# Optimization experiments

Hardware: AMD Instinct MI355X
Metric: run time of the kernel (lower is better)

The kernel has to match this reference:

```python
import jax, jax.numpy as jnp
import numpy as np
from jax import lax

D = 128          # dense volume side length
N = 500_000      # active voxels
CIN = 32
COUT = 32
K = 125          # 5x5x5 kernel taps
EPS = 1e-5       # BatchNorm eps (torch default)


def _build_sparse_grid():
    """Sample N unique voxels in a D^3 volume and build the [N, K] neighbor
    index table for a 5x5x5 stencil (-1 = neighbor not in the sparse grid)."""
    rng = np.random.default_rng(0)
    flat = rng.choice(D ** 3, size=N, replace=False).astype(np.int64)
    vol = np.full(D ** 3, -1, np.int32)
    vol[flat] = np.arange(N, dtype=np.int32)
    cz = flat % D
    cy = (flat // D) % D
    cx = flat // (D * D)
    coords = np.stack([cx, cy, cz], axis=1)
    nbr = np.empty((N, K), np.int32)
    k = 0
    for dx in range(-2, 3):
        for dy in range(-2, 3):
            for dz in range(-2, 3):
                c = coords + np.array([dx, dy, dz])
                ok = ((c >= 0) & (c < D)).all(axis=1)
                f = (c[:, 0] * D + c[:, 1]) * D + c[:, 2]
                nbr[:, k] = np.where(ok, vol[np.clip(f, 0, D ** 3 - 1)], -1)
                k += 1
    return nbr


def setup_inputs() -> dict:
    key = jax.random.key(0)
    ks = jax.random.split(key, 5)
    nbr = jnp.asarray(_build_sparse_grid())
    return {
        "x": jax.random.normal(ks[0], (N, CIN), jnp.float32),
        "nbr": nbr,
        "W_conv": jax.random.normal(ks[1], (K, CIN, COUT), jnp.float32) * 0.02,
        "b_conv": jax.random.normal(ks[2], (COUT,), jnp.float32) * 0.02,
        "gamma": jnp.ones((COUT,), jnp.float32),
        "beta": jnp.zeros((COUT,), jnp.float32),
        "W_lin": jax.random.normal(ks[3], (COUT, COUT), jnp.float32) * 0.02,
        "b_lin": jax.random.normal(ks[4], (COUT,), jnp.float32) * 0.02,
    }


def reference(x, nbr, W_conv, b_conv, gamma, beta, W_lin, b_lin):
    n = x.shape[0]

    # Sparse 5x5x5 conv: scan over the 125 kernel taps, gather neighbor
    # features (zero for missing neighbors) and accumulate tap GEMMs.
    def tap(acc, wi):
        w, idx = wi                              # w: [CIN, COUT], idx: [N]
        valid = (idx >= 0)[:, None]
        g = jnp.where(valid, x[jnp.maximum(idx, 0)], 0.0)  # [N, CIN]
        return acc + g @ w, None

    init = jnp.broadcast_to(b_conv, (n, b_conv.shape[0])).astype(x.dtype)
    out, _ = lax.scan(tap, init, (W_conv, nbr.T))

    # BatchNorm over all voxels (training-mode batch statistics, biased var)
    mean = out.mean(axis=0)
    var = out.var(axis=0)
    out = (out - mean) * lax.rsqrt(var + EPS) * gamma + beta

    # ELU (alpha=1.0), then pointwise SparseLinear
    out = jax.nn.elu(out)
    return out @ W_lin.T + b_lin
```

## Files before the change

### kernel.cpp

```cpp
#include <hip/hip_runtime.h>
#include <stdint.h>


#define NV 500000
#define KT 125
#define CH 32
#define EPSBN 1e-5f
#define NTILES (NV / 16)

typedef __attribute__((ext_vector_type(8))) short short8;
typedef __attribute__((ext_vector_type(4))) float f32x4;

__device__ __forceinline__ unsigned short f2bf(float f) {
    union { float f; unsigned int u; } v; v.f = f;
    unsigned int u = v.u;
    return (unsigned short)((u + 0x7fffu + ((u >> 16) & 1u)) >> 16);
}

__global__ __launch_bounds__(256) void
k_prep(const float* __restrict__ x, const float* __restrict__ Wc,
       const float* __restrict__ Wlin,
       unsigned short* __restrict__ xb, unsigned short* __restrict__ wf,
       unsigned short* __restrict__ wl, float* __restrict__ stats) {
    int tid = blockIdx.x * blockDim.x + threadIdx.x;
    if (blockIdx.x == 0 && threadIdx.x < 64) stats[threadIdx.x] = 0.0f;
    if (tid < KT * 2 * 64) {
        int k = tid >> 7;
        int rem = tid & 127;
        int h = rem >> 6;
        int l = rem & 63;
        int kd0 = (l >> 4) * 8;
        int cc = h * 16 + (l & 15);
        #pragma unroll
        for (int j = 0; j < 8; j++)
            wf[tid * 8 + j] = f2bf(Wc[(k * CH + kd0 + j) * CH + cc]);
    } else if (tid < KT * 2 * 64 + 128) {
        int t2 = tid - KT * 2 * 64;
        int h = t2 >> 6;
        int l = t2 & 63;
        int n = l & 15;
        int kd0 = (l >> 4) * 8;
        #pragma unroll
        for (int j = 0; j < 8; j++)
            wl[t2 * 8 + j] = f2bf(Wlin[(h * 16 + n) * CH + kd0 + j]);
    }
    size_t i8 = (size_t)tid * 8;
    if (i8 < (size_t)NV * CH) {
        float4 a = *(const float4*)(x + i8);
        float4 b = *(const float4*)(x + i8 + 4);
        short8 o;
        o[0] = (short)f2bf(a.x); o[1] = (short)f2bf(a.y);
        o[2] = (short)f2bf(a.z); o[3] = (short)f2bf(a.w);
        o[4] = (short)f2bf(b.x); o[5] = (short)f2bf(b.y);
        o[6] = (short)f2bf(b.z); o[7] = (short)f2bf(b.w);
        *(short8*)(xb + i8) = o;
    }
}


__device__ __forceinline__ void
load_nb(int w, const int* __restrict__ nbr, const int (&rbase)[4], int q, int (&out)[4][4]) {
    #pragma unroll
    for (int t = 0; t < 4; t++) {
        #pragma unroll
        for (int r = 0; r < 4; r++) {
            int k = w * 16 + r * 4 + q;
            out[t][r] = nbr[rbase[t] + (k > 124 ? 124 : k)];
        }
    }
}

template<int BANK, int C0>
__device__ __forceinline__ void
refill(short8 (&A)[2][2][4], short8 (&B)[2][2][2], int k0, const int (&nb)[4][4],
       const unsigned short* __restrict__ xb, const unsigned short* __restrict__ wf,
       int m, int q, int lane) {
    #pragma unroll
    for (int jj = 0; jj < 2; jj++) {
        const int c = C0 + jj;
        int k = k0 + jj;
        int kc = k > 124 ? 124 : k;
        B[BANK][jj][0] = *(const short8*)(wf + (size_t)(kc * 128 + lane) * 8);
        B[BANK][jj][1] = *(const short8*)(wf + (size_t)(kc * 128 + 64 + lane) * 8);
        #pragma unroll
        for (int t = 0; t < 4; t++) {
            int idx = __shfl(nb[t][c >> 2], ((c & 3) << 4) | m, 64);
            if (k > 124) idx = -1;
            short8 a = {0, 0, 0, 0, 0, 0, 0, 0};
            if (idx >= 0) a = *(const short8*)(xb + (size_t)idx * CH + q * 8);
            A[BANK][jj][t] = a;
        }
    }
}

template<int BANK>
__device__ __forceinline__ void
consume(f32x4 (&acc)[4][2], const short8 (&A)[2][2][4], const short8 (&B)[2][2][2]) {
    #pragma unroll
    for (int jj = 0; jj < 2; jj++) {
        #pragma unroll
        for (int t = 0; t < 4; t++) {
            acc[t][0] = __builtin_amdgcn_mfma_f32_16x16x32_bf16(A[BANK][jj][t], B[BANK][jj][0], acc[t][0], 0, 0, 0);
            acc[t][1] = __builtin_amdgcn_mfma_f32_16x16x32_bf16(A[BANK][jj][t], B[BANK][jj][1], acc[t][1], 0, 0, 0);
        }
    }
}

__global__ __launch_bounds__(256, 2) void
k_conv(const unsigned short* __restrict__ xb, const int* __restrict__ nbr,
       const unsigned short* __restrict__ wf, float* __restrict__ co,
       float* __restrict__ stats) {
    const int lane = threadIdx.x & 63;
    const int wv = threadIdx.x >> 6;
    const int m = lane & 15;
    const int q = lane >> 4;
    const int vbase = (blockIdx.x * 4 + wv) * 64;

    f32x4 acc[4][2];
    #pragma unroll
    for (int t = 0; t < 4; t++)
        for (int h = 0; h < 2; h++)
            acc[t][h] = f32x4{0.f, 0.f, 0.f, 0.f};

    bool tval[4];
    int rbase[4];
    #pragma unroll
    for (int t = 0; t < 4; t++) {
        tval[t] = (vbase + t * 16) < NV;
        rbase[t] = tval[t] ? (vbase + t * 16 + m) * KT : 0;
    }

    short8 A[2][2][4];
    short8 B[2][2][2];
    int nb[4][4], nbn[4][4];

    load_nb(0, nbr, rbase, q, nb);
    refill<0, 0>(A, B, 0, nb, xb, wf, m, q, lane);
    refill<1, 2>(A, B, 2, nb, xb, wf, m, q, lane);

    for (int w = 0; w < 8; w++) {
        const int kb = w * 16;
        if (w < 7) load_nb(w + 1, nbr, rbase, q, nbn);
        consume<0>(acc, A, B); refill<0, 4>(A, B, kb + 4, nb, xb, wf, m, q, lane);
        consume<1>(acc, A, B); refill<1, 6>(A, B, kb + 6, nb, xb, wf, m, q, lane);
        consume<0>(acc, A, B); refill<0, 8>(A, B, kb + 8, nb, xb, wf, m, q, lane);
        consume<1>(acc, A, B); refill<1, 10>(A, B, kb + 10, nb, xb, wf, m, q, lane);
        consume<0>(acc, A, B); refill<0, 12>(A, B, kb + 12, nb, xb, wf, m, q, lane);
        consume<1>(acc, A, B); refill<1, 14>(A, B, kb + 14, nb, xb, wf, m, q, lane);
        consume<0>(acc, A, B); refill<0, 0>(A, B, kb + 16, nbn, xb, wf, m, q, lane);
        consume<1>(acc, A, B); refill<1, 2>(A, B, kb + 18, nbn, xb, wf, m, q, lane);
        #pragma unroll
        for (int t = 0; t < 4; t++)
            #pragma unroll
            for (int r = 0; r < 4; r++)
                nb[t][r] = nbn[t][r];
    }

    float s0 = 0.f, s1 = 0.f, q0 = 0.f, q1 = 0.f;
    #pragma unroll
    for (int t = 0; t < 4; t++) {
        if (!tval[t]) continue;
        int v0 = vbase + t * 16 + q * 4;
        #pragma unroll
        for (int r = 0; r < 4; r++) {
            float a0 = acc[t][0][r], a1 = acc[t][1][r];
            co[(size_t)(v0 + r) * CH + m] = a0;
            co[(size_t)(v0 + r) * CH + 16 + m] = a1;
            s0 += a0; q0 += a0 * a0;
            s1 += a1; q1 += a1 * a1;
        }
    }
    s0 += __shfl_xor(s0, 16); s0 += __shfl_xor(s0, 32);
    s1 += __shfl_xor(s1, 16); s1 += __shfl_xor(s1, 32);
    q0 += __shfl_xor(q0, 16); q0 += __shfl_xor(q0, 32);
    q1 += __shfl_xor(q1, 16); q1 += __shfl_xor(q1, 32);
    if (q == 0) {
        atomicAdd(&stats[m],      s0);
        atomicAdd(&stats[16 + m], s1);
        atomicAdd(&stats[32 + m], q0);
        atomicAdd(&stats[48 + m], q1);
    }
}

__global__ void k_final(const float* __restrict__ gamma, const float* __restrict__ beta,
                        float* __restrict__ stats) {
    int c = threadIdx.x;
    if (c < CH) {
        float mean = stats[c] * (1.0f / NV);
        float var = stats[32 + c] * (1.0f / NV) - mean * mean;
        float sc = gamma[c] * rsqrtf(var + EPSBN);
        stats[64 + c] = sc;
        stats[96 + c] = beta[c] - mean * sc;
    }
}

__global__ __launch_bounds__(256) void
k_epi(float* __restrict__ io, const unsigned short* __restrict__ wl,
      const float* __restrict__ blin, const float* __restrict__ stats) {
    const int lane = threadIdx.x & 63;
    const int wv = threadIdx.x >> 6;
    const int m = lane & 15;
    const int q = lane >> 4;

    short8 wl0 = *(const short8*)(wl + (size_t)lane * 8);
    short8 wl1 = *(const short8*)(wl + (size_t)(64 + lane) * 8);
    float ssc8[8], ssh8[8];
    #pragma unroll
    for (int j = 0; j < 8; j++) {
        ssc8[j] = stats[64 + q * 8 + j];
        ssh8[j] = stats[96 + q * 8 + j];
    }
    float bias0 = blin[m];
    float bias1 = blin[16 + m];

    const int wstep = gridDim.x * 4;
    for (int tile = blockIdx.x * 4 + wv; tile < NTILES; tile += wstep) {
        const int v0 = tile * 16;
        const float* p = io + (size_t)(v0 + m) * CH + q * 8;
        float4 e0 = *(const float4*)p;
        float4 e1 = *(const float4*)(p + 4);
        float e[8] = {e0.x, e0.y, e0.z, e0.w, e1.x, e1.y, e1.z, e1.w};
        short8 a;
        #pragma unroll
        for (int j = 0; j < 8; j++) {
            float f = e[j] * ssc8[j] + ssh8[j];
            f = f > 0.0f ? f : (__expf(f) - 1.0f);
            a[j] = (short)f2bf(f);
        }
        f32x4 z = {0.f, 0.f, 0.f, 0.f};
        f32x4 d0 = __builtin_amdgcn_mfma_f32_16x16x32_bf16(a, wl0, z, 0, 0, 0);
        f32x4 d1 = __builtin_amdgcn_mfma_f32_16x16x32_bf16(a, wl1, z, 0, 0, 0);
        #pragma unroll
        for (int r = 0; r < 4; r++) {
            io[(size_t)(v0 + q * 4 + r) * CH + m]      = d0[r] + bias0;
            io[(size_t)(v0 + q * 4 + r) * CH + 16 + m] = d1[r] + bias1;
        }
    }
}

extern "C" void kernel_launch(void* const* d_in, const int* in_sizes, int n_in,
                              void* d_out, int out_size, void* d_ws, size_t ws_size,
                              hipStream_t stream) {
    const float* x     = (const float*)d_in[0];
    const int*   nbr   = (const int*)d_in[1];
    const float* Wc    = (const float*)d_in[2];
    const float* gamma = (const float*)d_in[4];
    const float* beta  = (const float*)d_in[5];
    const float* Wlin  = (const float*)d_in[6];
    const float* blin  = (const float*)d_in[7];
    float* out = (float*)d_out;

    char* ws = (char*)d_ws;
    unsigned short* xb = (unsigned short*)ws;
    size_t off = (size_t)NV * CH * 2;
    unsigned short* wf = (unsigned short*)(ws + off);
    off += (size_t)KT * 128 * 8 * 2;
    unsigned short* wl = (unsigned short*)(ws + off);
    off += 128 * 8 * 2;
    float* stats = (float*)(ws + off);

    int prep_blocks = (int)(((size_t)NV * CH / 8 + 255) / 256);
    hipLaunchKernelGGL(k_prep, dim3(prep_blocks), dim3(256), 0, stream,
                       x, Wc, Wlin, xb, wf, wl, stats);
    hipLaunchKernelGGL(k_conv, dim3((NV + 255) / 256), dim3(256), 0, stream,
                       xb, nbr, wf, out, stats);
    hipLaunchKernelGGL(k_final, dim3(1), dim3(64), 0, stream, gamma, beta, stats);
    hipLaunchKernelGGL(k_epi, dim3(1024), dim3(256), 0, stream, out, wl, blin, stats);
}
```

Baseline: 739.9 us.

## Gather neighbor rows directly into LDS with async global_load_lds pipeline

Replaces the register-based gather of neighbor feature rows with global_load_lds copies into a 4-slot per-wave LDS ring, using a zero page in global memory for missing neighbors instead of predicated loads. Neighbor indices are now fetched as vectorized int4 loads. An explicit vmcnt wait paces a three-stage-deep prefetch. The aim is to keep more gather loads in flight and cut VGPR pressure. In exchange it uses 128 KB of LDS per block, which limits occupancy to one block per CU, and the launch bound drops its two-blocks hint.

```diff
diff --git a/kernel.cpp b/kernel.cpp
--- a/kernel.cpp
+++ b/kernel.cpp
@@ -10,6 +10,7 @@
 
 typedef __attribute__((ext_vector_type(8))) short short8;
 typedef __attribute__((ext_vector_type(4))) float f32x4;
+typedef __attribute__((ext_vector_type(4), aligned(4))) int int4a;
 
 __device__ __forceinline__ unsigned short f2bf(float f) {
     union { float f; unsigned int u; } v; v.f = f;
@@ -17,13 +18,23 @@
     return (unsigned short)((u + 0x7fffu + ((u >> 16) & 1u)) >> 16);
 }
 
+__device__ __forceinline__ void gload_lds16(const void* g, void* l) {
+    __builtin_amdgcn_global_load_lds(
+        (const __attribute__((address_space(1))) unsigned int*)g,
+        (__attribute__((address_space(3))) unsigned int*)l, 16, 0, 0);
+}
+
 __global__ __launch_bounds__(256) void
 k_prep(const float* __restrict__ x, const float* __restrict__ Wc,
        const float* __restrict__ Wlin,
        unsigned short* __restrict__ xb, unsigned short* __restrict__ wf,
-       unsigned short* __restrict__ wl, float* __restrict__ stats) {
+       unsigned short* __restrict__ wl, float* __restrict__ stats,
+       float* __restrict__ zpg) {
     int tid = blockIdx.x * blockDim.x + threadIdx.x;
-    if (blockIdx.x == 0 && threadIdx.x < 64) stats[threadIdx.x] = 0.0f;
+    if (blockIdx.x == 0 && threadIdx.x < 96) {
+        if (threadIdx.x < 64) stats[threadIdx.x] = 0.0f;
+        else                  zpg[threadIdx.x - 64] = 0.0f;
+    }
     if (tid < KT * 2 * 64) {
         int k = tid >> 7;
         int rem = tid & 127;
@@ -57,68 +68,73 @@
     }
 }
 
-
-__device__ __forceinline__ void
-load_nb(int w, const int* __restrict__ nbr, const int (&rbase)[4], int q, int (&out)[4][4]) {
-    #pragma unroll
-    for (int t = 0; t < 4; t++) {
-        #pragma unroll
-        for (int r = 0; r < 4; r++) {
-            int k = w * 16 + r * 4 + q;
-            out[t][r] = nbr[rbase[t] + (k > 124 ? 124 : k)];
-        }
-    }
-}
-
-template<int BANK, int C0>
-__device__ __forceinline__ void
-refill(short8 (&A)[2][2][4], short8 (&B)[2][2][2], int k0, const int (&nb)[4][4],
-       const unsigned short* __restrict__ xb, const unsigned short* __restrict__ wf,
-       int m, int q, int lane) {
-    #pragma unroll
-    for (int jj = 0; jj < 2; jj++) {
-        const int c = C0 + jj;
-        int k = k0 + jj;
-        int kc = k > 124 ? 124 : k;
-        B[BANK][jj][0] = *(const short8*)(wf + (size_t)(kc * 128 + lane) * 8);
-        B[BANK][jj][1] = *(const short8*)(wf + (size_t)(kc * 128 + 64 + lane) * 8);
-        #pragma unroll
-        for (int t = 0; t < 4; t++) {
-            int idx = __shfl(nb[t][c >> 2], ((c & 3) << 4) | m, 64);
-            if (k > 124) idx = -1;
-            short8 a = {0, 0, 0, 0, 0, 0, 0, 0};
-            if (idx >= 0) a = *(const short8*)(xb + (size_t)idx * CH + q * 8);
-            A[BANK][jj][t] = a;
-        }
-    }
-}
-
-template<int BANK>
-__device__ __forceinline__ void
-consume(f32x4 (&acc)[4][2], const short8 (&A)[2][2][4], const short8 (&B)[2][2][2]) {
-    #pragma unroll
-    for (int jj = 0; jj < 2; jj++) {
-        #pragma unroll
-        for (int t = 0; t < 4; t++) {
-            acc[t][0] = __builtin_amdgcn_mfma_f32_16x16x32_bf16(A[BANK][jj][t], B[BANK][jj][0], acc[t][0], 0, 0, 0);
-            acc[t][1] = __builtin_amdgcn_mfma_f32_16x16x32_bf16(A[BANK][jj][t], B[BANK][jj][1], acc[t][1], 0, 0, 0);
-        }
-    }
-}
-
-__global__ __launch_bounds__(256, 2) void
+#define GATHER8(SLOT, C0, KG, NBARR)                                          \
+    do {                                                                      \
+        _Pragma("unroll")                                                     \
+        for (int jj = 0; jj < 2; jj++) {                                      \
+            const int c_ = (C0) + jj;                                         \
+            const int k_ = (KG) + jj;                                         \
+            _Pragma("unroll")                                                 \
+            for (int t_ = 0; t_ < 4; t_++) {                                  \
+                int idx_ = __shfl(NBARR[t_][c_ & 3], ((c_ >> 2) << 4) | m, 64); \
+                const char* src_ = xbB + ((size_t)(unsigned)idx_ << 6) + q16; \
+                if ((idx_ < 0) || (k_ > 124)) src_ = zpgB + q16;              \
+                gload_lds16(src_, lds_wb + (SLOT) * 8192 + (jj * 4 + t_) * 1024); \
+            }                                                                 \
+        }                                                                     \
+    } while (0)
+
+#define BODY(P, SRC, W, WL)                                                   \
+    do {                                                                      \
+        if ((P) < 4)                                                          \
+            nbn4[(P) & 3] = *(const int4a*)(nbr + rbase[(P) & 3] + (WL) * 16 + q4); \
+        GATHER8(((P) + 3) & 3, (2 * ((P) + 3)) & 15, ((W) * 8 + (P) + 3) * 2, SRC); \
+        {                                                                     \
+            const int bk_ = ((P) + 1) & 1;                                    \
+            const int kg_ = ((W) * 8 + (P) + 1) * 2;                          \
+            _Pragma("unroll")                                                 \
+            for (int jj = 0; jj < 2; jj++) {                                  \
+                int kc_ = kg_ + jj; if (kc_ > 124) kc_ = 124;                 \
+                Bf[bk_][jj][0] = *(const short8*)(wf + (size_t)(kc_ * 128 + lane) * 8); \
+                Bf[bk_][jj][1] = *(const short8*)(wf + (size_t)(kc_ * 128 + 64 + lane) * 8); \
+            }                                                                 \
+        }                                                                     \
+        asm volatile("s_waitcnt vmcnt(24)" ::: "memory");                     \
+        {                                                                     \
+            _Pragma("unroll")                                                 \
+            for (int jj = 0; jj < 2; jj++) {                                  \
+                _Pragma("unroll")                                             \
+                for (int t_ = 0; t_ < 4; t_++) {                              \
+                    short8 a_ = *(const short8*)(lds_lane + ((P) & 3) * 8192 + (jj * 4 + t_) * 1024); \
+                    acc[t_][0] = __builtin_amdgcn_mfma_f32_16x16x32_bf16(a_, Bf[(P) & 1][jj][0], acc[t_][0], 0, 0, 0); \
+                    acc[t_][1] = __builtin_amdgcn_mfma_f32_16x16x32_bf16(a_, Bf[(P) & 1][jj][1], acc[t_][1], 0, 0, 0); \
+                }                                                             \
+            }                                                                 \
+        }                                                                     \
+    } while (0)
+
+__global__ __launch_bounds__(256) void
 k_conv(const unsigned short* __restrict__ xb, const int* __restrict__ nbr,
        const unsigned short* __restrict__ wf, float* __restrict__ co,
-       float* __restrict__ stats) {
+       float* __restrict__ stats, const float* __restrict__ zpg) {
     const int lane = threadIdx.x & 63;
     const int wv = threadIdx.x >> 6;
     const int m = lane & 15;
     const int q = lane >> 4;
+    const int q4 = q * 4;
+    const int q16 = q * 16;
     const int vbase = (blockIdx.x * 4 + wv) * 64;
 
+    __shared__ __attribute__((aligned(128))) char smem[131072];
+    char* lds_wb = smem + wv * 32768;
+    const char* lds_lane = lds_wb + lane * 16;
+    const char* xbB = (const char*)xb;
+    const char* zpgB = (const char*)zpg;
+
     f32x4 acc[4][2];
     #pragma unroll
     for (int t = 0; t < 4; t++)
+        #pragma unroll
         for (int h = 0; h < 2; h++)
             acc[t][h] = f32x4{0.f, 0.f, 0.f, 0.f};
 
@@ -130,30 +146,37 @@
         rbase[t] = tval[t] ? (vbase + t * 16 + m) * KT : 0;
     }
 
-    short8 A[2][2][4];
-    short8 B[2][2][2];
-    int nb[4][4], nbn[4][4];
-
-    load_nb(0, nbr, rbase, q, nb);
-    refill<0, 0>(A, B, 0, nb, xb, wf, m, q, lane);
-    refill<1, 2>(A, B, 2, nb, xb, wf, m, q, lane);
+    short8 Bf[2][2][2];
+    int4a nb4[4], nbn4[4];
+
+    #pragma unroll
+    for (int t = 0; t < 4; t++)
+        nb4[t] = *(const int4a*)(nbr + rbase[t] + q4);
+
+    GATHER8(0, 0, 0, nb4);
+    asm volatile("" ::: "memory");
+    GATHER8(1, 2, 2, nb4);
+    asm volatile("" ::: "memory");
+    GATHER8(2, 4, 4, nb4);
+    asm volatile("" ::: "memory");
+    #pragma unroll
+    for (int jj = 0; jj < 2; jj++) {
+        Bf[0][jj][0] = *(const short8*)(wf + (size_t)(jj * 128 + lane) * 8);
+        Bf[0][jj][1] = *(const short8*)(wf + (size_t)(jj * 128 + 64 + lane) * 8);
+    }
 
     for (int w = 0; w < 8; w++) {
-        const int kb = w * 16;
-        if (w < 7) load_nb(w + 1, nbr, rbase, q, nbn);
-        consume<0>(acc, A, B); refill<0, 4>(A, B, kb + 4, nb, xb, wf, m, q, lane);
-        consume<1>(acc, A, B); refill<1, 6>(A, B, kb + 6, nb, xb, wf, m, q, lane);
-        consume<0>(acc, A, B); refill<0, 8>(A, B, kb + 8, nb, xb, wf, m, q, lane);
-        consume<1>(acc, A, B); refill<1, 10>(A, B, kb + 10, nb, xb, wf, m, q, lane);
-        consume<0>(acc, A, B); refill<0, 12>(A, B, kb + 12, nb, xb, wf, m, q, lane);
-        consume<1>(acc, A, B); refill<1, 14>(A, B, kb + 14, nb, xb, wf, m, q, lane);
-        consume<0>(acc, A, B); refill<0, 0>(A, B, kb + 16, nbn, xb, wf, m, q, lane);
-        consume<1>(acc, A, B); refill<1, 2>(A, B, kb + 18, nbn, xb, wf, m, q, lane);
-        #pragma unroll
-        for (int t = 0; t < 4; t++)
-            #pragma unroll
-            for (int r = 0; r < 4; r++)
-                nb[t][r] = nbn[t][r];
+        const int wl2 = (w < 7) ? w + 1 : 0;
+        BODY(0, nb4,  w, wl2);
+        BODY(1, nb4,  w, wl2);
+        BODY(2, nb4,  w, wl2);
+        BODY(3, nb4,  w, wl2);
+        BODY(4, nb4,  w, wl2);
+        BODY(5, nbn4, w, wl2);
+        BODY(6, nbn4, w, wl2);
+        BODY(7, nbn4, w, wl2);
+        #pragma unroll
+        for (int t = 0; t < 4; t++) nb4[t] = nbn4[t];
     }
 
     float s0 = 0.f, s1 = 0.f, q0 = 0.f, q1 = 0.f;
@@ -258,12 +281,14 @@
     unsigned short* wl = (unsigned short*)(ws + off);
     off += 128 * 8 * 2;
     float* stats = (float*)(ws + off);
+    off += 512;
+    float* zpg = (float*)(ws + off);
 
     int prep_blocks = (int)(((size_t)NV * CH / 8 + 255) / 256);
     hipLaunchKernelGGL(k_prep, dim3(prep_blocks), dim3(256), 0, stream,
-                       x, Wc, Wlin, xb, wf, wl, stats);
+                       x, Wc, Wlin, xb, wf, wl, stats, zpg);
     hipLaunchKernelGGL(k_conv, dim3((NV + 255) / 256), dim3(256), 0, stream,
-                       xb, nbr, wf, out, stats);
+                       xb, nbr, wf, out, stats, zpg);
     hipLaunchKernelGGL(k_final, dim3(1), dim3(64), 0, stream, gamma, beta, stats);
     hipLaunchKernelGGL(k_epi, dim3(1024), dim3(256), 0, stream, out, wl, blin, stats);
 }
```

Result: slower. 815.1 us (+10.2%).
